# Kernel optimization log

Measured on AMD Instinct MI355X. Metric: run time of the kernel, lower is better.

The kernel has to match this reference:

```python
import jax, jax.numpy as jnp
import numpy as np

D_MODEL = 1024
N_HEADS = 16
HEAD_DIM = D_MODEL // N_HEADS
N_SCALES = 11
_D4 = jnp.array([0.4829629131445341, 0.8365163037378079, 0.2241438680420134, -0.1294095225512604], dtype=jnp.float32)


def setup_inputs() -> dict:
    key = jax.random.key(0)
    ks = jax.random.split(key, 8)
    B, N, D = 8, 2048, D_MODEL
    s = 1.0 / np.sqrt(D)
    x = jax.random.normal(ks[0], (B, N, D), dtype=jnp.float32)
    qkv_w = jax.random.normal(ks[1], (3 * D, D), dtype=jnp.float32) * s
    qkv_b = jnp.zeros((3 * D,), dtype=jnp.float32)
    out_w = jax.random.normal(ks[2], (D, D), dtype=jnp.float32) * s
    out_b = jnp.zeros((D,), dtype=jnp.float32)
    gate_w = jax.random.normal(ks[3], (D, D), dtype=jnp.float32) * s
    gate_b = jnp.full((D,), 2.0, dtype=jnp.float32)  # nn.init.constant_(gate_proj.bias, 2.0)
    scale_gain = jax.random.normal(ks[4], (N_SCALES, N_HEADS), dtype=jnp.float32) * 0.1
    field_coupling = jnp.eye(N_HEADS, dtype=jnp.float32) + 0.01 * jax.random.normal(ks[5], (N_HEADS, N_HEADS), dtype=jnp.float32)
    return {"x": x, "qkv_w": qkv_w, "qkv_b": qkv_b, "out_w": out_w, "out_b": out_b,
            "gate_w": gate_w, "gate_b": gate_b, "scale_gain": scale_gain,
            "field_coupling": field_coupling}


def _causal_multiscale(x_c, scale_gain):
    # x_c: [B, C, N] with channel order (head-major, then head_dim)
    B, C, N = x_c.shape
    gains = jax.nn.softmax(scale_gain, axis=0)              # [S, H]
    gains_exp = jnp.repeat(gains, HEAD_DIM, axis=1)         # [S, C]
    out = jnp.zeros_like(x_c)
    for j in range(N_SCALES):
        d = 1 << j
        xp = jnp.pad(x_c, ((0, 0), (0, 0), (3 * d, 0)))     # causal left pad
        # depthwise dilated conv (cross-correlation, same D4 taps per channel)
        y = (_D4[0] * xp[:, :, 0 * d:0 * d + N]
             + _D4[1] * xp[:, :, 1 * d:1 * d + N]
             + _D4[2] * xp[:, :, 2 * d:2 * d + N]
             + _D4[3] * xp[:, :, 3 * d:3 * d + N])
        out = out + gains_exp[j][None, :, None] * y
    return out


def reference(x, qkv_w, qkv_b, out_w, out_b, gate_w, gate_b, scale_gain, field_coupling):
    B, N, D = x.shape
    H, HD = N_HEADS, HEAD_DIM
    qkv = x @ qkv_w.T + qkv_b                               # [B, N, 3D]
    q, k, v = jnp.split(qkv, 3, axis=-1)                    # q is unused (as in source)
    k = k.reshape(B, N, H, HD)
    v = v.reshape(B, N, H, HD)
    k_mag = jnp.linalg.norm(k, axis=-1, keepdims=True)      # [B, N, H, 1]
    field = v * k_mag                                       # [B, N, H, HD]
    # -> [B, C, N], C = H*HD, head-major channel layout
    x_c = jnp.transpose(field, (0, 2, 3, 1)).reshape(B, H * HD, N)
    out_c = _causal_multiscale(x_c, scale_gain)             # [B, C, N]
    field = out_c.reshape(B, H, HD, N)                      # [B, H, HD, N]
    coupling = jax.nn.softmax(field_coupling, axis=-1)      # [H, H]
    field = jnp.einsum('ij,bjdn->bidn', coupling, field)    # head coupling
    gathered = jnp.transpose(field, (0, 3, 1, 2)).reshape(B, N, D)
    gate = jax.nn.sigmoid(x @ gate_w.T + gate_b)
    return (gathered * gate) @ out_w.T + out_b
```

## Files before the change

kernel.cpp:

```cpp
#include <hip/hip_runtime.h>
#include <hip/hip_bf16.h>
#include <math.h>

#define BD 8
#define SN 2048
#define DM 1024
#define NH 16
#define HD 64
#define NS 11
#define NTAP 24
#define PAD 3072

typedef __attribute__((ext_vector_type(8))) short short8;
typedef __attribute__((ext_vector_type(4))) float floatx4;

__constant__ int OFFS[NTAP] = {0, 1, 2, 3, 4, 6, 8, 12, 16, 24, 32, 48, 64, 96,
                               128, 192, 256, 384, 512, 768, 1024, 1536, 2048, 3072};

__device__ __forceinline__ void async_load16(const void* g, void* lds) {
    __builtin_amdgcn_global_load_lds(
        (const __attribute__((address_space(1))) void*)g,
        (__attribute__((address_space(3))) void*)lds,
        16, 0, 0);
}

__global__ __launch_bounds__(256) void f2bf_kernel(const float* __restrict__ src,
                                                   __hip_bfloat16* __restrict__ dst,
                                                   int n4) {
    int i = blockIdx.x * 256 + threadIdx.x;
    if (i < n4) {
        const float4 v = reinterpret_cast<const float4*>(src)[i];
        union { __hip_bfloat16 h[4]; uint2 u; } cv;
        cv.h[0] = __float2bfloat16(v.x);
        cv.h[1] = __float2bfloat16(v.y);
        cv.h[2] = __float2bfloat16(v.z);
        cv.h[3] = __float2bfloat16(v.w);
        reinterpret_cast<uint2*>(dst)[i] = cv.u;
    }
}

__global__ void prep_kernel(const float* __restrict__ scale_gain,
                            const float* __restrict__ field_coupling,
                            const float* __restrict__ qkv_b,
                            const float* __restrict__ gate_b,
                            float* __restrict__ wtab,
                            float* __restrict__ cw,
                            float* __restrict__ biascat)
{
    const float D4[4] = {0.4829629131445341f, 0.8365163037378079f,
                         0.2241438680420134f, -0.1294095225512604f};
    int t = threadIdx.x;
    if (t < NH) {
        float g[NS];
        float m = -1e30f;
        for (int j = 0; j < NS; ++j) m = fmaxf(m, scale_gain[j * NH + t]);
        float s = 0.f;
        for (int j = 0; j < NS; ++j) { g[j] = expf(scale_gain[j * NH + t] - m); s += g[j]; }
        float inv = 1.f / s;
        for (int j = 0; j < NS; ++j) g[j] *= inv;
        for (int i = 0; i < NTAP; ++i) {
            float w = 0.f;
            for (int j = 0; j < NS; ++j)
                for (int tt = 0; tt < 4; ++tt)
                    if (((3 - tt) << j) == OFFS[i]) w += g[j] * D4[tt];
            wtab[i * NH + t] = w;
        }
    } else if (t < 2 * NH) {
        int r = t - NH;
        float m = -1e30f;
        for (int j = 0; j < NH; ++j) m = fmaxf(m, field_coupling[r * NH + j]);
        float e[NH]; float s = 0.f;
        for (int j = 0; j < NH; ++j) { e[j] = expf(field_coupling[r * NH + j] - m); s += e[j]; }
        float inv = 1.f / s;
        for (int j = 0; j < NH; ++j) cw[r * NH + j] = e[j] * inv;
    }
    for (int i = t; i < 2048; i += 256)
        biascat[i] = (i < 1024) ? qkv_b[1024 + i] : gate_b[i - 1024];
}

__global__ __launch_bounds__(256, 3) void gemm128_kernel(
    const __hip_bfloat16* __restrict__ A,
    const __hip_bfloat16* __restrict__ Bw,
    void* __restrict__ Cout,
    const float* __restrict__ bias,
    float* __restrict__ kmag,
    int M, int Nn, int K, int mode) {
    __shared__ short As[128 * 64];
    __shared__ short Bs[128 * 64];

    const int tid = threadIdx.x;
    const int m0 = blockIdx.y * 128;
    const int n0 = blockIdx.x * 128;
    const int wv = tid >> 6;
    const int ln = tid & 63;

    const int srow = ln >> 3;
    const int scc  = (ln & 7) ^ srow;
    size_t goffA[4], goffB[4];
    #pragma unroll
    for (int i = 0; i < 4; ++i) {
        const int row = wv * 32 + i * 8 + srow;
        goffA[i] = (size_t)(m0 + row) * K + scc * 8;
        goffB[i] = (size_t)(n0 + row) * K + scc * 8;
    }

    const int lrow = ln & 15, quad = ln >> 4;
    const int wm = (wv >> 1) * 64;
    const int wn = (wv & 1) * 64;
    int aaddr[4], baddr[4];
    #pragma unroll
    for (int t = 0; t < 4; ++t) {
        const int sw = (quad ^ (lrow & 7)) * 16;
        aaddr[t] = (wm + t * 16 + lrow) * 128 + sw;
        baddr[t] = (wn + t * 16 + lrow) * 128 + sw;
    }

    floatx4 acc[4][4];
    #pragma unroll
    for (int a = 0; a < 4; ++a)
        #pragma unroll
        for (int b = 0; b < 4; ++b) acc[a][b] = (floatx4){0.f, 0.f, 0.f, 0.f};

    for (int kt = 0; kt < K; kt += 64) {
        #pragma unroll
        for (int i = 0; i < 4; ++i) {
            async_load16(A + goffA[i] + kt, &As[(wv * 32 + i * 8) * 64]);
            async_load16(Bw + goffB[i] + kt, &Bs[(wv * 32 + i * 8) * 64]);
        }
        __syncthreads();
        #pragma unroll
        for (int h = 0; h < 2; ++h) {
            short8 a[4], b[4];
            #pragma unroll
            for (int t = 0; t < 4; ++t) {
                a[t] = *reinterpret_cast<const short8*>(
                           reinterpret_cast<const char*>(As) + (aaddr[t] ^ (h * 64)));
                b[t] = *reinterpret_cast<const short8*>(
                           reinterpret_cast<const char*>(Bs) + (baddr[t] ^ (h * 64)));
            }
            #pragma unroll
            for (int mt = 0; mt < 4; ++mt)
                #pragma unroll
                for (int nt = 0; nt < 4; ++nt)
                    acc[mt][nt] = __builtin_amdgcn_mfma_f32_16x16x32_bf16(
                        a[mt], b[nt], acc[mt][nt], 0, 0, 0);
        }
        __syncthreads();
    }

    if (mode == 2 && n0 < 1024) {
        const int h = (n0 + wn) >> 6;
        #pragma unroll
        for (int mt = 0; mt < 4; ++mt) {
            #pragma unroll
            for (int i = 0; i < 4; ++i) {
                float ss = 0.f;
                #pragma unroll
                for (int nt = 0; nt < 4; ++nt) {
                    const float v = acc[mt][nt][i] + bias[n0 + wn + nt * 16 + lrow];
                    ss += v * v;
                }
                ss += __shfl_xor(ss, 1);
                ss += __shfl_xor(ss, 2);
                ss += __shfl_xor(ss, 4);
                ss += __shfl_xor(ss, 8);
                if (lrow == 0) {
                    const int r = m0 + wm + mt * 16 + quad * 4 + i;
                    kmag[h * (BD * SN) + r] = sqrtf(ss);
                }
            }
        }
        return;
    }

    #pragma unroll
    for (int mt = 0; mt < 4; ++mt) {
        #pragma unroll
        for (int nt = 0; nt < 4; ++nt) {
            const int col = n0 + wn + nt * 16 + lrow;
            float bv = 0.f;
            if (bias && mode != 1) bv = bias[col];
            #pragma unroll
            for (int i = 0; i < 4; ++i) {
                const int row = m0 + wm + mt * 16 + quad * 4 + i;
                float val = acc[mt][nt][i] + bv;
                if (mode == 1 && bias) val += bias[row];
                if (mode == 0) {
                    ((float*)Cout)[(size_t)row * Nn + col] = val;
                } else if (mode == 1) {
                    ((__hip_bfloat16*)Cout)[(size_t)row * Nn + col] = __float2bfloat16(val);
                } else {
                    val = 1.f / (1.f + expf(-val));
                    ((__hip_bfloat16*)Cout)[(size_t)row * 1024 + (col - 1024)] =
                        __float2bfloat16(val);
                }
            }
        }
    }
}

__global__ __launch_bounds__(256) void wavelet_kernel(const __hip_bfloat16* __restrict__ fieldv,
                                                      const float* __restrict__ kmag,
                                                      const float* __restrict__ wtab,
                                                      __hip_bfloat16* __restrict__ wave) {
    const int bc = blockIdx.x;
    const int b = bc >> 10;
    const int c = bc & (DM - 1);
    const int h = c >> 6;
    __shared__ float row[PAD + SN];
    __shared__ float wt[NTAP];
    const __hip_bfloat16* src = fieldv + (size_t)c * (BD * SN) + b * SN;
    const float* mag = kmag + (size_t)h * (BD * SN) + b * SN;
    const int t = threadIdx.x;
    for (int i = t; i < PAD; i += 256) row[i] = 0.f;
    for (int i = t; i < SN; i += 256)
        row[PAD + i] = __bfloat162float(src[i]) * mag[i];
    if (t < NTAP) wt[t] = wtab[t * NH + h];
    __syncthreads();
    __hip_bfloat16* dst = wave + (size_t)bc * SN;
    for (int n = t; n < SN; n += 256) {
        const float* base = &row[PAD + n];
        float acc = 0.f;
        #pragma unroll
        for (int i = 0; i < NTAP; ++i) acc += wt[i] * base[-OFFS[i]];
        dst[n] = __float2bfloat16(acc);
    }
}

__global__ __launch_bounds__(256) void couple_kernel(const __hip_bfloat16* __restrict__ wave,
                                                     const float* __restrict__ cw,
                                                     __hip_bfloat16* __restrict__ cpl) {
    const int b = blockIdx.z, d = blockIdx.y;
    const int n = blockIdx.x * 256 + threadIdx.x;
    __shared__ float w[256];
    w[threadIdx.x] = cw[threadIdx.x];
    __syncthreads();
    size_t base = (size_t)b * DM * SN + (size_t)d * SN + n;
    float r[NH];
    #pragma unroll
    for (int hi = 0; hi < NH; ++hi) r[hi] = __bfloat162float(wave[base + (size_t)hi * 64 * SN]);
    #pragma unroll
    for (int ho = 0; ho < NH; ++ho) {
        float acc = 0.f;
        #pragma unroll
        for (int hi = 0; hi < NH; ++hi) acc += w[ho * 16 + hi] * r[hi];
        cpl[base + (size_t)ho * 64 * SN] = __float2bfloat16(acc);
    }
}

__global__ __launch_bounds__(256) void transgate_kernel(const __hip_bfloat16* __restrict__ cpl,
                                                        const __hip_bfloat16* __restrict__ gate,
                                                        __hip_bfloat16* __restrict__ Ag) {
    const int b = blockIdx.z;
    const int c0 = blockIdx.y * 64, n0 = blockIdx.x * 64;
    __shared__ float tile[64][65];
    const int t = threadIdx.x;
    #pragma unroll
    for (int i = 0; i < 16; ++i) {
        int idx = t + i * 256;
        int ci = idx >> 6, nj = idx & 63;
        tile[ci][nj] = __bfloat162float(cpl[((size_t)b * DM + c0 + ci) * SN + n0 + nj]);
    }
    __syncthreads();
    #pragma unroll
    for (int i = 0; i < 16; ++i) {
        int idx = t + i * 256;
        int nj = idx >> 6, ci = idx & 63;
        size_t off = ((size_t)(b * SN + n0 + nj)) * DM + c0 + ci;
        Ag[off] = __float2bfloat16(tile[ci][nj] * __bfloat162float(gate[off]));
    }
}

extern "C" void kernel_launch(void* const* d_in, const int* in_sizes, int n_in,
                              void* d_out, int out_size, void* d_ws, size_t ws_size,
                              hipStream_t stream) {
    const float* x     = (const float*)d_in[0];
    const float* qkv_w = (const float*)d_in[1];
    const float* qkv_b = (const float*)d_in[2];
    const float* out_w = (const float*)d_in[3];
    const float* out_b = (const float*)d_in[4];
    const float* gate_w = (const float*)d_in[5];
    const float* gate_b = (const float*)d_in[6];
    const float* scale_gain = (const float*)d_in[7];
    const float* field_coupling = (const float*)d_in[8];

    char* ws = (char*)d_ws;
    const int M = BD * SN;

    __hip_bfloat16* x_bf    = (__hip_bfloat16*)(ws);
    __hip_bfloat16* wkg_bf  = (__hip_bfloat16*)(ws + 33554432);
    __hip_bfloat16* wv_bf   = (__hip_bfloat16*)(ws + 37748736);
    __hip_bfloat16* wo_bf   = (__hip_bfloat16*)(ws + 39845888);
    float* wtab             = (float*)(ws + 41943040);
    float* cwbuf            = (float*)(ws + 41944576);
    float* biascat          = (float*)(ws + 41945600);
    float* kmag             = (float*)(ws + 41953792);
    __hip_bfloat16* fieldv  = (__hip_bfloat16*)(ws + 43002368);
    __hip_bfloat16* gate_bf = (__hip_bfloat16*)(ws + 76556800);
    __hip_bfloat16* wave_bf = (__hip_bfloat16*)(ws + 110111232);
    __hip_bfloat16* cpl_bf = fieldv;
    __hip_bfloat16* Ag     = x_bf;
    float* out = (float*)d_out;

    f2bf_kernel<<<(M * DM / 4 + 255) / 256, 256, 0, stream>>>(x, x_bf, M * DM / 4);
    f2bf_kernel<<<(DM * DM / 4 + 255) / 256, 256, 0, stream>>>(qkv_w + (size_t)DM * DM, wkg_bf, DM * DM / 4);
    f2bf_kernel<<<(DM * DM / 4 + 255) / 256, 256, 0, stream>>>(gate_w, wkg_bf + (size_t)DM * DM, DM * DM / 4);
    f2bf_kernel<<<(DM * DM / 4 + 255) / 256, 256, 0, stream>>>(qkv_w + (size_t)2 * DM * DM, wv_bf, DM * DM / 4);
    f2bf_kernel<<<(DM * DM / 4 + 255) / 256, 256, 0, stream>>>(out_w, wo_bf, DM * DM / 4);

    prep_kernel<<<1, 256, 0, stream>>>(scale_gain, field_coupling, qkv_b, gate_b,
                                       wtab, cwbuf, biascat);

    {
        dim3 grid(2 * DM / 128, M / 128);
        gemm128_kernel<<<grid, 256, 0, stream>>>(x_bf, wkg_bf, gate_bf, biascat, kmag,
                                                 M, 2 * DM, DM, 2);
    }
    {
        dim3 grid(M / 128, DM / 128);
        gemm128_kernel<<<grid, 256, 0, stream>>>(wv_bf, x_bf, fieldv, qkv_b + 2 * DM, nullptr,
                                                 DM, M, DM, 1);
    }
    wavelet_kernel<<<BD * DM, 256, 0, stream>>>(fieldv, kmag, wtab, wave_bf);
    {
        dim3 grid(SN / 256, HD, BD);
        couple_kernel<<<grid, 256, 0, stream>>>(wave_bf, cwbuf, cpl_bf);
    }
    {
        dim3 grid(SN / 64, DM / 64, BD);
        transgate_kernel<<<grid, 256, 0, stream>>>(cpl_bf, gate_bf, Ag);
    }
    {
        dim3 grid(DM / 128, M / 128);
        gemm128_kernel<<<grid, 256, 0, stream>>>(Ag, wo_bf, out, out_b, nullptr,
                                                 M, DM, DM, 0);
    }
}
```

Before: 409.4 us.

## Fuse head coupling with transpose-gate and vectorize wavelet convolution

Merges the couple and transgate kernels into one kernel that loads a 1024-channel by 32-position tile of the wavelet output into LDS with async loads, applies the 16x16 head-coupling matrix in registers, transposes through swizzled LDS and multiplies by the gate. This removes a full bf16 intermediate round trip through global memory and one launch. The wavelet kernel also switches to vectorized loads, register-held tap weights and four outputs per thread using float4 LDS reads. The fused kernel uses about 66KB of LDS and many registers, which limits occupancy.

```diff
diff --git a/kernel.cpp b/kernel.cpp
--- a/kernel.cpp
+++ b/kernel.cpp
@@ -14,14 +14,26 @@
 typedef __attribute__((ext_vector_type(8))) short short8;
 typedef __attribute__((ext_vector_type(4))) float floatx4;
 
-__constant__ int OFFS[NTAP] = {0, 1, 2, 3, 4, 6, 8, 12, 16, 24, 32, 48, 64, 96,
-                               128, 192, 256, 384, 512, 768, 1024, 1536, 2048, 3072};
+constexpr int OFFS[NTAP] = {0, 1, 2, 3, 4, 6, 8, 12, 16, 24, 32, 48, 64, 96,
+                            128, 192, 256, 384, 512, 768, 1024, 1536, 2048, 3072};
 
 __device__ __forceinline__ void async_load16(const void* g, void* lds) {
     __builtin_amdgcn_global_load_lds(
         (const __attribute__((address_space(1))) void*)g,
         (__attribute__((address_space(3))) void*)lds,
         16, 0, 0);
+}
+
+__device__ __forceinline__ float bf2f(int v) {
+    union { unsigned u; float f; } cv;
+    cv.u = ((unsigned)v & 0xffffu) << 16;
+    return cv.f;
+}
+
+__device__ __forceinline__ unsigned short f2bfbits(float x) {
+    union { __hip_bfloat16 h; unsigned short u; } cv;
+    cv.h = __float2bfloat16(x);
+    return cv.u;
 }
 
 __global__ __launch_bounds__(256) void f2bf_kernel(const float* __restrict__ src,
@@ -208,66 +220,142 @@
     const int c = bc & (DM - 1);
     const int h = c >> 6;
     __shared__ float row[PAD + SN];
-    __shared__ float wt[NTAP];
-    const __hip_bfloat16* src = fieldv + (size_t)c * (BD * SN) + b * SN;
-    const float* mag = kmag + (size_t)h * (BD * SN) + b * SN;
     const int t = threadIdx.x;
-    for (int i = t; i < PAD; i += 256) row[i] = 0.f;
-    for (int i = t; i < SN; i += 256)
-        row[PAD + i] = __bfloat162float(src[i]) * mag[i];
-    if (t < NTAP) wt[t] = wtab[t * NH + h];
+
+    float w[NTAP];
+    #pragma unroll
+    for (int i = 0; i < NTAP; ++i) w[i] = wtab[i * NH + h];
+
+    {
+        float4* r4 = reinterpret_cast<float4*>(row);
+        const float4 zv = {0.f, 0.f, 0.f, 0.f};
+        #pragma unroll
+        for (int i = 0; i < 3; ++i) r4[t + i * 256] = zv;
+    }
+    {
+        const __hip_bfloat16* src = fieldv + (size_t)c * (BD * SN) + b * SN;
+        const float* mag = kmag + (size_t)h * (BD * SN) + b * SN;
+        const int i = t * 8;
+        const short8 s = *reinterpret_cast<const short8*>(src + i);
+        const float4 m0 = *reinterpret_cast<const float4*>(mag + i);
+        const float4 m1 = *reinterpret_cast<const float4*>(mag + i + 4);
+        float4 o0, o1;
+        o0.x = bf2f(s[0]) * m0.x; o0.y = bf2f(s[1]) * m0.y;
+        o0.z = bf2f(s[2]) * m0.z; o0.w = bf2f(s[3]) * m0.w;
+        o1.x = bf2f(s[4]) * m1.x; o1.y = bf2f(s[5]) * m1.y;
+        o1.z = bf2f(s[6]) * m1.z; o1.w = bf2f(s[7]) * m1.w;
+        *reinterpret_cast<float4*>(&row[PAD + i]) = o0;
+        *reinterpret_cast<float4*>(&row[PAD + i + 4]) = o1;
+    }
     __syncthreads();
+
     __hip_bfloat16* dst = wave + (size_t)bc * SN;
-    for (int n = t; n < SN; n += 256) {
-        const float* base = &row[PAD + n];
-        float acc = 0.f;
-        #pragma unroll
-        for (int i = 0; i < NTAP; ++i) acc += wt[i] * base[-OFFS[i]];
-        dst[n] = __float2bfloat16(acc);
-    }
-}
-
-__global__ __launch_bounds__(256) void couple_kernel(const __hip_bfloat16* __restrict__ wave,
-                                                     const float* __restrict__ cw,
-                                                     __hip_bfloat16* __restrict__ cpl) {
-    const int b = blockIdx.z, d = blockIdx.y;
-    const int n = blockIdx.x * 256 + threadIdx.x;
-    __shared__ float w[256];
-    w[threadIdx.x] = cw[threadIdx.x];
+    #pragma unroll
+    for (int pass = 0; pass < 2; ++pass) {
+        const int n = (pass * 256 + t) * 4;
+        const float* bp = &row[PAD + n];
+        const float4 qc = *reinterpret_cast<const float4*>(bp);
+        const float4 qb = *reinterpret_cast<const float4*>(bp - 4);
+        const float4 qa = *reinterpret_cast<const float4*>(bp - 8);
+        float a0, a1, a2, a3;
+        a0 = w[0] * qc.x; a1 = w[0] * qc.y; a2 = w[0] * qc.z; a3 = w[0] * qc.w;
+        a0 += w[1] * qb.w; a1 += w[1] * qc.x; a2 += w[1] * qc.y; a3 += w[1] * qc.z;
+        a0 += w[2] * qb.z; a1 += w[2] * qb.w; a2 += w[2] * qc.x; a3 += w[2] * qc.y;
+        a0 += w[3] * qb.y; a1 += w[3] * qb.z; a2 += w[3] * qb.w; a3 += w[3] * qc.x;
+        a0 += w[4] * qb.x; a1 += w[4] * qb.y; a2 += w[4] * qb.z; a3 += w[4] * qb.w;
+        a0 += w[5] * qa.z; a1 += w[5] * qa.w; a2 += w[5] * qb.x; a3 += w[5] * qb.y;
+        a0 += w[6] * qa.x; a1 += w[6] * qa.y; a2 += w[6] * qa.z; a3 += w[6] * qa.w;
+        #pragma unroll
+        for (int i = 7; i < NTAP; ++i) {
+            const float4 q = *reinterpret_cast<const float4*>(bp - OFFS[i]);
+            a0 += w[i] * q.x; a1 += w[i] * q.y; a2 += w[i] * q.z; a3 += w[i] * q.w;
+        }
+        union { __hip_bfloat16 hh[4]; uint2 u; } cv;
+        cv.hh[0] = __float2bfloat16(a0); cv.hh[1] = __float2bfloat16(a1);
+        cv.hh[2] = __float2bfloat16(a2); cv.hh[3] = __float2bfloat16(a3);
+        *reinterpret_cast<uint2*>(dst + n) = cv.u;
+    }
+}
+
+__global__ __launch_bounds__(256) void couplegate_kernel(
+        const __hip_bfloat16* __restrict__ wave,
+        const float* __restrict__ cw,
+        const __hip_bfloat16* __restrict__ gate,
+        __hip_bfloat16* __restrict__ Ag) {
+    const int b = blockIdx.y;
+    const int n0 = blockIdx.x * 32;
+    __shared__ unsigned short U[33 * 1024];
+    __shared__ float cwl[NH * NH];
+    const int t = threadIdx.x;
+    const int wv = t >> 6, ln = t & 63;
+
+    #pragma unroll
+    for (int p = 0; p < 16; ++p) {
+        const int u = p * 256 + wv * 64 + ln;
+        const int cch = u >> 2, qs = u & 3;
+        const int qg = qs ^ (cch & 3);
+        async_load16(wave + (size_t)(b * DM + cch) * SN + n0 + qg * 8,
+                     (char*)U + (size_t)(p * 256 + wv * 64) * 16);
+    }
+    cwl[t] = cw[t];
     __syncthreads();
-    size_t base = (size_t)b * DM * SN + (size_t)d * SN + n;
-    float r[NH];
-    #pragma unroll
-    for (int hi = 0; hi < NH; ++hi) r[hi] = __bfloat162float(wave[base + (size_t)hi * 64 * SN]);
-    #pragma unroll
-    for (int ho = 0; ho < NH; ++ho) {
-        float acc = 0.f;
-        #pragma unroll
-        for (int hi = 0; hi < NH; ++hi) acc += w[ho * 16 + hi] * r[hi];
-        cpl[base + (size_t)ho * 64 * SN] = __float2bfloat16(acc);
-    }
-}
-
-__global__ __launch_bounds__(256) void transgate_kernel(const __hip_bfloat16* __restrict__ cpl,
-                                                        const __hip_bfloat16* __restrict__ gate,
-                                                        __hip_bfloat16* __restrict__ Ag) {
-    const int b = blockIdx.z;
-    const int c0 = blockIdx.y * 64, n0 = blockIdx.x * 64;
-    __shared__ float tile[64][65];
-    const int t = threadIdx.x;
-    #pragma unroll
-    for (int i = 0; i < 16; ++i) {
-        int idx = t + i * 256;
-        int ci = idx >> 6, nj = idx & 63;
-        tile[ci][nj] = __bfloat162float(cpl[((size_t)b * DM + c0 + ci) * SN + n0 + nj]);
+
+    const int nq = t & 7;
+    const int d0 = t >> 3;
+    const int d1 = 32 + d0;
+    float v0[16][4], v1[16][4];
+    #pragma unroll
+    for (int hi = 0; hi < 16; ++hi) {
+        #pragma unroll
+        for (int q = 0; q < 4; ++q) {
+            const int s0 = q ^ (d0 & 3);
+            const int s1 = q ^ (d1 & 3);
+            v0[hi][q] = bf2f(U[(hi * 64 + d0) * 32 + s0 * 8 + nq]);
+            v1[hi][q] = bf2f(U[(hi * 64 + d1) * 32 + s1 * 8 + nq]);
+        }
     }
     __syncthreads();
-    #pragma unroll
-    for (int i = 0; i < 16; ++i) {
-        int idx = t + i * 256;
-        int nj = idx >> 6, ci = idx & 63;
-        size_t off = ((size_t)(b * SN + n0 + nj)) * DM + c0 + ci;
-        Ag[off] = __float2bfloat16(tile[ci][nj] * __bfloat162float(gate[off]));
+
+    #pragma unroll
+    for (int ho = 0; ho < 16; ++ho) {
+        float cwr[16];
+        #pragma unroll
+        for (int j = 0; j < 4; ++j) {
+            const float4 c4 = *reinterpret_cast<const float4*>(&cwl[ho * 16 + j * 4]);
+            cwr[j * 4 + 0] = c4.x; cwr[j * 4 + 1] = c4.y;
+            cwr[j * 4 + 2] = c4.z; cwr[j * 4 + 3] = c4.w;
+        }
+        float a0[4] = {0.f, 0.f, 0.f, 0.f}, a1[4] = {0.f, 0.f, 0.f, 0.f};
+        #pragma unroll
+        for (int hi = 0; hi < 16; ++hi) {
+            #pragma unroll
+            for (int q = 0; q < 4; ++q) {
+                a0[q] += cwr[hi] * v0[hi][q];
+                a1[q] += cwr[hi] * v1[hi][q];
+            }
+        }
+        #pragma unroll
+        for (int q = 0; q < 4; ++q) {
+            const int nloc = q * 8 + nq;
+            U[nloc * 1032 + ho * 64 + d0] = f2bfbits(a0[q]);
+            U[nloc * 1032 + ho * 64 + d1] = f2bfbits(a1[q]);
+        }
+    }
+    __syncthreads();
+
+    #pragma unroll
+    for (int p = 0; p < 16; ++p) {
+        const int idx = p * 256 + t;
+        const int nloc = idx >> 7, cu = idx & 127;
+        const short8 ov = *reinterpret_cast<const short8*>(&U[nloc * 1032 + cu * 8]);
+        const size_t off = ((size_t)(b * SN + n0 + nloc)) * DM + cu * 8;
+        const short8 gv = *reinterpret_cast<const short8*>(
+            reinterpret_cast<const unsigned short*>(gate) + off);
+        union { __hip_bfloat16 hh[8]; short8 s; } cv;
+        #pragma unroll
+        for (int j = 0; j < 8; ++j)
+            cv.hh[j] = __float2bfloat16(bf2f(ov[j]) * bf2f(gv[j]));
+        *reinterpret_cast<short8*>(reinterpret_cast<unsigned short*>(Ag) + off) = cv.s;
     }
 }
 
@@ -298,8 +386,7 @@
     __hip_bfloat16* fieldv  = (__hip_bfloat16*)(ws + 43002368);
     __hip_bfloat16* gate_bf = (__hip_bfloat16*)(ws + 76556800);
     __hip_bfloat16* wave_bf = (__hip_bfloat16*)(ws + 110111232);
-    __hip_bfloat16* cpl_bf = fieldv;
-    __hip_bfloat16* Ag     = x_bf;
+    __hip_bfloat16* Ag = x_bf;
     float* out = (float*)d_out;
 
     f2bf_kernel<<<(M * DM / 4 + 255) / 256, 256, 0, stream>>>(x, x_bf, M * DM / 4);
@@ -323,12 +410,8 @@
     }
     wavelet_kernel<<<BD * DM, 256, 0, stream>>>(fieldv, kmag, wtab, wave_bf);
     {
-        dim3 grid(SN / 256, HD, BD);
-        couple_kernel<<<grid, 256, 0, stream>>>(wave_bf, cwbuf, cpl_bf);
-    }
-    {
-        dim3 grid(SN / 64, DM / 64, BD);
-        transgate_kernel<<<grid, 256, 0, stream>>>(cpl_bf, gate_bf, Ag);
+        dim3 grid(SN / 32, BD);
+        couplegate_kernel<<<grid, 256, 0, stream>>>(wave_bf, cwbuf, gate_bf, Ag);
     }
     {
         dim3 grid(DM / 128, M / 128);
```

Measured after the change: 400.0 us. 1.02x faster.
